# Optimization experiments

Hardware: AMD Instinct MI355X
Metric: run time of the kernel (lower is better)

Reference implementation:

```python
import jax, jax.numpy as jnp
import numpy as np

COMMITMENT = 1.0


def setup_inputs() -> dict:
    key = jax.random.key(0)
    k1, k2 = jax.random.split(key)
    input = jax.random.normal(k1, (8, 64, 64, 256), dtype=jnp.float32)
    embed = jax.random.normal(k2, (256, 8192), dtype=jnp.float32)  # [dim, n_embed]
    return {"input": input, "embed": embed}


def reference(input, embed):
    dim = embed.shape[0]
    flatten = input.reshape(-1, dim)  # [N, dim]
    dist = (
        jnp.sum(flatten * flatten, axis=1, keepdims=True)
        - 2.0 * (flatten @ embed)
        + jnp.sum(embed * embed, axis=0, keepdims=True)
    )
    embed_ind = jnp.argmin(dist, axis=1)  # == (-dist).max(1) indices
    embed_ind = embed_ind.reshape(input.shape[:-1])  # [B, H, W]
    quantize = jnp.take(embed.T, embed_ind, axis=0)  # codebook lookup [B,H,W,dim]
    loss = jnp.mean((jax.lax.stop_gradient(quantize) - input) ** 2) * COMMITMENT
    quantize = input + jax.lax.stop_gradient(quantize - input)  # straight-through
    return quantize, embed_ind, loss
```

## Files before the change

kernel.cpp:

```cpp
#include <hip/hip_runtime.h>
#include <hip/hip_fp16.h>

#define NROW 32768
#define DIM  256
#define NC   8192
#define CAP  16384
#define MARGINF 0.25f
#define BIAS 512.0f
#define AST 576
#define BST 576
#define LOSS_SCALE (1.0f / 8388608.0f)

typedef __attribute__((ext_vector_type(8))) _Float16 half8;
typedef __attribute__((ext_vector_type(4))) _Float16 half4;
typedef __attribute__((ext_vector_type(4))) float   floatx4;
typedef const __attribute__((address_space(1))) void* gas_p;
typedef __attribute__((address_space(3))) void*       las_p;

static __device__ __forceinline__ unsigned short f2hb(float f) {
    _Float16 h = (_Float16)f;
    unsigned short u;
    __builtin_memcpy(&u, &h, 2);
    return u;
}
static __device__ __forceinline__ unsigned umin_(unsigned a, unsigned b) { return a < b ? a : b; }
static __device__ __forceinline__ unsigned umax_(unsigned a, unsigned b) { return a > b ? a : b; }


__global__ void prep_a_k(const float* __restrict__ x, unsigned short* __restrict__ Ah,
                         float* __restrict__ norms) {
    int row  = blockIdx.x * 4 + (threadIdx.x >> 6);
    int lane = threadIdx.x & 63;
    const float4 v = ((const float4*)(x + (size_t)row * DIM))[lane];
    float s = v.x * v.x + v.y * v.y + v.z * v.z + v.w * v.w;
#pragma unroll
    for (int off = 32; off; off >>= 1) s += __shfl_down(s, off, 64);
    if (lane == 0) norms[row] = s;
    ushort4 hi4 = make_ushort4(f2hb(v.x), f2hb(v.y), f2hb(v.z), f2hb(v.w));
    ushort4 lo4 = make_ushort4(f2hb(v.x - (float)(_Float16)v.x),
                               f2hb(v.y - (float)(_Float16)v.y),
                               f2hb(v.z - (float)(_Float16)v.z),
                               f2hb(v.w - (float)(_Float16)v.w));
    unsigned short* rp = Ah + (size_t)row * AST;
    *(ushort4*)(rp + lane * 4)       = hi4;
    *(ushort4*)(rp + 288 + lane * 4) = lo4;
    if (lane < 8) {
        ushort4 ob = make_ushort4(0, 0, 0, 0);
        if (lane == 0) { ob.x = 0x3C00; ob.y = 0x3C00; }
        *(ushort4*)(rp + 256 + lane * 4) = ob;
    }
}

__global__ void code_norms_k(const float* __restrict__ e, unsigned short* __restrict__ Bh,
                             float* __restrict__ cHalf) {
    int j = blockIdx.x * 256 + threadIdx.x;
    float s = 0.f;
    for (int d = 0; d < DIM; ++d) { float v = e[(size_t)d * NC + j]; s += v * v; }
    cHalf[j] = 0.5f * s;
    float t = -0.5f * s - BIAS;
    unsigned short hi = f2hb(t);
    _Float16 hf; __builtin_memcpy(&hf, &hi, 2);
    unsigned short lo = f2hb(t - (float)hf);
    unsigned short* p = Bh + (size_t)j * BST + 256;
    p[0] = hi; p[1] = lo;
    for (int k2 = 2; k2 < 32; ++k2) p[k2] = 0;
}

__global__ void prep_b_k(const float* __restrict__ e, unsigned short* __restrict__ Bh) {
    __shared__ float t[32][33];
    int jb = blockIdx.x * 32, db = blockIdx.y * 32;
#pragma unroll
    for (int i = 0; i < 4; ++i)
        t[threadIdx.y + i * 8][threadIdx.x] =
            e[(size_t)(db + threadIdx.y + i * 8) * NC + jb + threadIdx.x];
    __syncthreads();
#pragma unroll
    for (int i = 0; i < 4; ++i) {
        int j = jb + threadIdx.y + i * 8;
        int d = db + threadIdx.x;
        float val = t[threadIdx.x][threadIdx.y + i * 8];
        Bh[(size_t)j * BST + d]       = f2hb(val);
        Bh[(size_t)j * BST + 288 + d] = f2hb(val - (float)(_Float16)val);
    }
}


#define WAITBAR asm volatile("s_waitcnt vmcnt(2) lgkmcnt(4)\n\ts_barrier" ::: "memory")

__global__ __launch_bounds__(512, 2) void vq_cheap_k(
    const unsigned short* __restrict__ Ah, const unsigned short* __restrict__ Bh,
    const float* __restrict__ cHalf,
    float* __restrict__ pv, int* __restrict__ pj, float* __restrict__ psv)
{
    __shared__ __align__(16) _Float16 Asl[8][4096];
    __shared__ __align__(16) _Float16 Bsl[4][8192];
    __shared__ float chl[2048];

    const int tid  = threadIdx.x;
    const int js   = blockIdx.x & 3;
    const int rb   = blockIdx.x >> 2;
    const int row0 = rb * 128, col0 = js * 2048;
    const int lane = tid & 63, l15 = lane & 15, lq = lane >> 4;
    const int wave = tid >> 6;
    const int wr = (wave >> 2) * 64;
    const int wc = (wave & 3) * 64;
    const int sr = tid >> 2;
    const int ks = (((tid & 3) ^ (sr & 3) ^ ((sr >> 2) & 3))) * 8;

    {
        float4 a = ((const float4*)(cHalf + col0))[tid];
        a.x += BIAS; a.y += BIAS; a.z += BIAS; a.w += BIAS;
        ((float4*)chl)[tid] = a;
    }

    const unsigned short* Abase = Ah + (size_t)(row0 + sr) * AST + ks;
#pragma unroll
    for (int c = 0; c < 8; ++c)
        __builtin_amdgcn_global_load_lds((gas_p)(Abase + c * 32), (las_p)&Asl[c][tid * 8], 16, 0, 0);

#define LOADB(JT_, C_, BUF_)                                                                  \
    do {                                                                                      \
        const unsigned short* bb_ = Bh + (size_t)(col0 + (JT_) * 256 + sr) * BST + (C_) * 32 + ks; \
        _Float16* lb_ = &Bsl[(BUF_)][tid * 8];                                                \
        __builtin_amdgcn_global_load_lds((gas_p)bb_,               (las_p)lb_,          16, 0, 0); \
        __builtin_amdgcn_global_load_lds((gas_p)(bb_ + 128 * BST), (las_p)(lb_ + 4096), 16, 0, 0); \
    } while (0)

    LOADB(0, 0, 0);
    LOADB(0, 1, 1);
    LOADB(0, 2, 2);

    unsigned k1[16], k2[16];
#pragma unroll
    for (int s = 0; s < 16; ++s) { k1[s] = 0xFFFFFFFFu; k2[s] = 0xFFFFFFFFu; }

    const floatx4 fzero = {0.0f, 0.0f, 0.0f, 0.0f};
    floatx4 acc[4][4];
#pragma unroll
    for (int rf = 0; rf < 4; ++rf)
#pragma unroll
        for (int cf = 0; cf < 4; ++cf) acc[rf][cf] = fzero;

    WAITBAR;

    half8 ar[4][4];
#pragma unroll
    for (int c = 0; c < 4; ++c)
#pragma unroll
        for (int rf = 0; rf < 4; ++rf) {
            const int m = wr + rf * 16 + l15;
            const int g = lq ^ (m & 3) ^ ((m >> 2) & 3);
            ar[c][rf] = *(const half8*)&Asl[c][m * 32 + g * 8];
        }

    half8 af[4], bf[4];
#pragma unroll
    for (int cf = 0; cf < 4; ++cf) {
        const int n = wc + cf * 16 + l15;
        const int g = lq ^ (n & 3) ^ ((n >> 2) & 3);
        bf[cf] = *(const half8*)&Bsl[0][n * 32 + g * 8];
    }

    for (int jt = 0; jt < 8; ++jt) {
#pragma unroll
        for (int c = 0; c < 8; ++c) {
            if (c <= 4) LOADB(jt, c + 3, (c + 3) & 3);
            else        LOADB((jt + 1) & 7, c - 5, (c + 3) & 3);

            __builtin_amdgcn_s_setprio(1);
            if (c < 4) {
#pragma unroll
                for (int rf = 0; rf < 4; ++rf)
#pragma unroll
                    for (int cf = 0; cf < 4; ++cf)
                        acc[rf][cf] = __builtin_amdgcn_mfma_f32_16x16x32_f16(
                            ar[c][rf], bf[cf], acc[rf][cf], 0, 0, 0);
            } else {
#pragma unroll
                for (int rf = 0; rf < 4; ++rf)
#pragma unroll
                    for (int cf = 0; cf < 4; ++cf)
                        acc[rf][cf] = __builtin_amdgcn_mfma_f32_16x16x32_f16(
                            af[rf], bf[cf], acc[rf][cf], 0, 0, 0);
            }
            __builtin_amdgcn_s_setprio(0);
            __builtin_amdgcn_sched_barrier(0);

            if (c == 7) {
#pragma unroll
                for (int cf = 0; cf < 4; ++cf) {
                    const unsigned colb = (unsigned)(jt * 256 + wc + cf * 16 + l15);
                    const float ch = chl[colb];
#pragma unroll
                    for (int rf = 0; rf < 4; ++rf)
#pragma unroll
                        for (int r = 0; r < 4; ++r) {
                            float s = acc[rf][cf][r] - ch;
                            unsigned key = (__float_as_uint(s) & 0xFFFFF800u) | colb;
                            int slot = rf * 4 + r;
                            unsigned t = umax_(key, k1[slot]);
                            k1[slot] = umin_(k1[slot], key);
                            k2[slot] = umin_(k2[slot], t);
                        }
                }
#pragma unroll
                for (int rf = 0; rf < 4; ++rf)
#pragma unroll
                    for (int cf = 0; cf < 4; ++cf) acc[rf][cf] = fzero;
            }

            if (((c + 1) & 7) >= 4) {
#pragma unroll
                for (int rf = 0; rf < 4; ++rf) {
                    const int m = wr + rf * 16 + l15;
                    const int g = lq ^ (m & 3) ^ ((m >> 2) & 3);
                    af[rf] = *(const half8*)&Asl[(c + 1) & 7][m * 32 + g * 8];
                }
            }
#pragma unroll
            for (int cf = 0; cf < 4; ++cf) {
                const int n = wc + cf * 16 + l15;
                const int g = lq ^ (n & 3) ^ ((n >> 2) & 3);
                bf[cf] = *(const half8*)&Bsl[(c + 1) & 3][n * 32 + g * 8];
            }

            WAITBAR;
        }
    }
#undef LOADB

#pragma unroll
    for (int st = 1; st < 16; st <<= 1) {
#pragma unroll
        for (int s = 0; s < 16; ++s) {
            unsigned o1 = (unsigned)__shfl_xor((int)k1[s], st, 64);
            unsigned o2 = (unsigned)__shfl_xor((int)k2[s], st, 64);
            unsigned t = umax_(k1[s], o1);
            k1[s] = umin_(k1[s], o1);
            k2[s] = umin_(umin_(k2[s], o2), t);
        }
    }

    __syncthreads();
    unsigned* mk1 = (unsigned*)&Asl[0][0];
    unsigned* mk2 = (unsigned*)&Asl[1][0];
    if (l15 == 0) {
#pragma unroll
        for (int rf = 0; rf < 4; ++rf)
#pragma unroll
            for (int r = 0; r < 4; ++r) {
                int rloc = wr + rf * 16 + lq * 4 + r;
                int slot = rf * 4 + r;
                mk1[rloc * 4 + (wave & 3)] = k1[slot];
                mk2[rloc * 4 + (wave & 3)] = k2[slot];
            }
    }
    __syncthreads();
    if (tid < 128) {
        unsigned a0 = mk1[tid * 4], a1 = mk1[tid * 4 + 1], a2 = mk1[tid * 4 + 2], a3 = mk1[tid * 4 + 3];
        unsigned x = umin_(a0, a1), y = umax_(a0, a1);
        unsigned z = umin_(a2, a3), w = umax_(a2, a3);
        unsigned m1  = umin_(x, z);
        unsigned sm1 = umin_(umax_(x, z), umin_(y, w));
        unsigned s0 = mk2[tid * 4], s1 = mk2[tid * 4 + 1], s2 = mk2[tid * 4 + 2], s3 = mk2[tid * 4 + 3];
        unsigned m2 = umin_(umin_(umin_(s0, s1), umin_(s2, s3)), sm1);
        pv[(size_t)js * NROW + row0 + tid]  = __uint_as_float(m1 & 0xFFFFF800u);
        pj[(size_t)js * NROW + row0 + tid]  = (int)(m1 & 2047u) + js * 2048;
        psv[(size_t)js * NROW + row0 + tid] = __uint_as_float(m2 & 0xFFFFF800u);
    }
}

#undef WAITBAR


template<bool RESCUE>
static __device__ __forceinline__ void chunk_off(int c, int& ac, int& bc) {
    if constexpr (RESCUE) {
        if (c < 8)       { ac = c * 32;              bc = c * 32; }
        else if (c < 16) { ac = (c - 8) * 32;        bc = 288 + (c - 8) * 32; }
        else             { ac = 288 + (c - 16) * 32; bc = (c - 16) * 32; }
    } else {
        ac = c * 32; bc = c * 32;
    }
}

#define GWAIT asm volatile("s_waitcnt vmcnt(4) lgkmcnt(0)\n\ts_barrier" ::: "memory")

template<int CHUNKS, int JT, int JSB, bool RESCUE>
__global__ __launch_bounds__(256, 2) void vq_gemm_k(
    const unsigned short* __restrict__ Ah, const unsigned short* __restrict__ Bh,
    const float* __restrict__ cHalf,
    float* __restrict__ pv, int* __restrict__ pj, float* __restrict__ psv,
    const int* __restrict__ list, const int* __restrict__ cnt)
{
    static_assert(CHUNKS % 3 == 0, "3-deep ring requires CHUNKS % 3 == 0");
    __shared__ __align__(16) _Float16 As[3][4096];
    __shared__ __align__(16) _Float16 Bs[3][4096];

    const int tid  = threadIdx.x;
    const int js   = blockIdx.x & ((1 << JSB) - 1);
    const int rb   = blockIdx.x >> JSB;
    const int row0 = rb * 128, col0 = js * (JT * 128);
    const int lane = tid & 63, l15 = lane & 15, lq = lane >> 4;
    const int wave = tid >> 6;
    const int wrow = (wave >> 1) * 64, wcol = (wave & 1) * 64;
    const int sr = tid >> 2, sp = (tid & 3) * 8;

    int nact = 0;
    if constexpr (RESCUE) {
        nact = *cnt;
        if (row0 >= nact) return;
    }

    const unsigned short *Abase0, *Abase1;
    if constexpr (RESCUE) {
        int i0 = row0 + sr, i1 = i0 + 64;
        int r0 = (i0 < nact) ? list[i0] : 0;
        int r1 = (i1 < nact) ? list[i1] : 0;
        Abase0 = Ah + (size_t)r0 * AST + sp;
        Abase1 = Ah + (size_t)r1 * AST + sp;
    } else {
        Abase0 = Ah + (size_t)(row0 + sr) * AST + sp;
        Abase1 = Abase0 + 64 * AST;
    }

    unsigned k1[16], k2[16];
    float bvf[16]; int bjf[16];
#pragma unroll
    for (int s = 0; s < 16; ++s) {
        k1[s] = 0xFFFFFFFFu; k2[s] = 0xFFFFFFFFu;
        bvf[s] = -3.4e38f; bjf[s] = 0;
    }

    const floatx4 fzero = {0.0f, 0.0f, 0.0f, 0.0f};
    floatx4 acc[4][4];
#pragma unroll
    for (int rf = 0; rf < 4; ++rf)
#pragma unroll
        for (int cf = 0; cf < 4; ++cf) acc[rf][cf] = fzero;

    const unsigned short* Bb0 = Bh + (size_t)(col0 + sr) * BST + sp;

#define LOAD4T(JT_, C_)                                                                      \
    do {                                                                                     \
        int an_, bn_;                                                                        \
        chunk_off<RESCUE>((C_), an_, bn_);                                                   \
        const unsigned short* bb_ = Bb0 + (size_t)(JT_) * (128 * BST);                       \
        _Float16* la_ = &As[(C_) % 3][tid * 8];                                              \
        _Float16* lb_ = &Bs[(C_) % 3][tid * 8];                                              \
        __builtin_amdgcn_global_load_lds((gas_p)(Abase0 + an_),            (las_p)la_,          16, 0, 0); \
        __builtin_amdgcn_global_load_lds((gas_p)(Abase1 + an_),            (las_p)(la_ + 2048), 16, 0, 0); \
        __builtin_amdgcn_global_load_lds((gas_p)(bb_ + bn_),               (las_p)lb_,          16, 0, 0); \
        __builtin_amdgcn_global_load_lds((gas_p)(bb_ + 64 * BST + bn_),    (las_p)(lb_ + 2048), 16, 0, 0); \
    } while (0)

    LOAD4T(0, 0);
    LOAD4T(0, 1);

    for (int jt = 0; jt < JT; ++jt) {
#pragma unroll
        for (int c = 0; c < CHUNKS; ++c) {
            GWAIT;
            if (c + 2 < CHUNKS)       LOAD4T(jt, c + 2);
            else if (jt + 1 < JT)     LOAD4T(jt + 1, c + 2 - CHUNKS);

            half8 af[4], bf[4];
#pragma unroll
            for (int rf = 0; rf < 4; ++rf)
                af[rf] = *(const half8*)&As[c % 3][(wrow + rf * 16 + l15) * 32 + lq * 8];
#pragma unroll
            for (int cf = 0; cf < 4; ++cf)
                bf[cf] = *(const half8*)&Bs[c % 3][(wcol + cf * 16 + l15) * 32 + lq * 8];
#pragma unroll
            for (int rf = 0; rf < 4; ++rf)
#pragma unroll
                for (int cf = 0; cf < 4; ++cf)
                    acc[rf][cf] = __builtin_amdgcn_mfma_f32_16x16x32_f16(
                        af[rf], bf[cf], acc[rf][cf], 0, 0, 0);

            if (c == CHUNKS - 1) {
                if constexpr (RESCUE) {
                    const int colbase = col0 + jt * 128 + wcol;
#pragma unroll
                    for (int cf = 0; cf < 4; ++cf) {
                        const int col = colbase + cf * 16 + l15;
                        const float ch = cHalf[col];
#pragma unroll
                        for (int rf = 0; rf < 4; ++rf)
#pragma unroll
                            for (int r = 0; r < 4; ++r) {
                                float s = acc[rf][cf][r] - ch;
                                int slot = rf * 4 + r;
                                if (s > bvf[slot]) { bvf[slot] = s; bjf[slot] = col; }
                            }
                    }
                } else {
                    const unsigned colloc = (unsigned)(jt * 128 + wcol);
#pragma unroll
                    for (int cf = 0; cf < 4; ++cf) {
                        const unsigned colb = colloc + cf * 16 + l15;
#pragma unroll
                        for (int rf = 0; rf < 4; ++rf)
#pragma unroll
                            for (int r = 0; r < 4; ++r) {
                                unsigned key = (__float_as_uint(acc[rf][cf][r]) & 0xFFFFF800u) | colb;
                                int slot = rf * 4 + r;
                                unsigned t = umax_(key, k1[slot]);
                                k1[slot] = umin_(k1[slot], key);
                                k2[slot] = umin_(k2[slot], t);
                            }
                    }
                }
#pragma unroll
                for (int rf = 0; rf < 4; ++rf)
#pragma unroll
                    for (int cf = 0; cf < 4; ++cf) acc[rf][cf] = fzero;
            }
        }
    }
#undef LOAD4T

#pragma unroll
    for (int st = 1; st < 16; st <<= 1) {
#pragma unroll
        for (int s = 0; s < 16; ++s) {
            if constexpr (RESCUE) {
                float v2 = __shfl_xor(bvf[s], st, 64);
                int   j2 = __shfl_xor(bjf[s], st, 64);
                if (v2 > bvf[s] || (v2 == bvf[s] && j2 < bjf[s])) { bvf[s] = v2; bjf[s] = j2; }
            } else {
                unsigned o1 = (unsigned)__shfl_xor((int)k1[s], st, 64);
                unsigned o2 = (unsigned)__shfl_xor((int)k2[s], st, 64);
                unsigned t = umax_(k1[s], o1);
                k1[s] = umin_(k1[s], o1);
                k2[s] = umin_(umin_(k2[s], o2), t);
            }
        }
    }

    __syncthreads();
    if constexpr (RESCUE) {
        float* mv = (float*)&As[0][0];
        int*   mj = (int*)&Bs[0][0];
        if (l15 == 0) {
#pragma unroll
            for (int rf = 0; rf < 4; ++rf)
#pragma unroll
                for (int r = 0; r < 4; ++r) {
                    int rloc = wrow + rf * 16 + lq * 4 + r;
                    int slot = rf * 4 + r;
                    mv[rloc * 2 + (wave & 1)] = bvf[slot];
                    mj[rloc * 2 + (wave & 1)] = bjf[slot];
                }
        }
        __syncthreads();
        if (tid < 128) {
            float v0 = mv[tid * 2], v1 = mv[tid * 2 + 1];
            int   j0 = mj[tid * 2], j1 = mj[tid * 2 + 1];
            bool take1 = (v1 > v0) || (v1 == v0 && j1 < j0);
            pv[(size_t)js * CAP + row0 + tid] = take1 ? v1 : v0;
            pj[(size_t)js * CAP + row0 + tid] = take1 ? j1 : j0;
        }
    } else {
        unsigned* mk1 = (unsigned*)&As[0][0];
        unsigned* mk2 = (unsigned*)&Bs[0][0];
        if (l15 == 0) {
#pragma unroll
            for (int rf = 0; rf < 4; ++rf)
#pragma unroll
                for (int r = 0; r < 4; ++r) {
                    int rloc = wrow + rf * 16 + lq * 4 + r;
                    int slot = rf * 4 + r;
                    mk1[rloc * 2 + (wave & 1)] = k1[slot];
                    mk2[rloc * 2 + (wave & 1)] = k2[slot];
                }
        }
        __syncthreads();
        if (tid < 128) {
            unsigned a1 = mk1[tid * 2], b1 = mk1[tid * 2 + 1];
            unsigned a2 = mk2[tid * 2], b2 = mk2[tid * 2 + 1];
            unsigned m1 = umin_(a1, b1);
            unsigned m2 = umin_(umin_(a2, b2), umax_(a1, b1));
            pv[(size_t)js * NROW + row0 + tid] = __uint_as_float(m1 & 0xFFFFF800u);
            pj[(size_t)js * NROW + row0 + tid] = (int)(m1 & 2047u) + js * (JT * 128);
            psv[(size_t)js * NROW + row0 + tid] = __uint_as_float(m2 & 0xFFFFF800u);
        }
    }
}


__global__ void vq_reduce_k(const float* __restrict__ pv, const int* __restrict__ pj,
                            const float* __restrict__ psv,
                            const float* __restrict__ norms, const unsigned short* __restrict__ Bh,
                            float* __restrict__ qout, float* __restrict__ iout,
                            float* __restrict__ lout, int* __restrict__ list,
                            int* __restrict__ cnt)
{
    __shared__ int jbuf[64];
    const int row0 = blockIdx.x * 64;
    const int tid = threadIdx.x;
    if (tid < 64) {
        int row = row0 + tid;
        float bv = pv[row]; int bj = pj[row]; float sv = psv[row];
#pragma unroll
        for (int s = 1; s < 4; ++s) {
            float v = pv[(size_t)s * NROW + row];
            int   j = pj[(size_t)s * NROW + row];
            float s2 = psv[(size_t)s * NROW + row];
            bool better = (v > bv) || (v == bv && j < bj);
            float loseBest = better ? bv : v;
            sv = fmaxf(fmaxf(sv, s2), loseBest);
            if (better) { bv = v; bj = j; }
        }
        bool flagged = (bv - sv) < MARGINF;
        if (flagged) {
            int idx = atomicAdd(cnt, 1);
            if (idx < CAP) {
                list[idx] = row;
                jbuf[tid] = -1;
            } else {
                flagged = false;
            }
        }
        float rl = 0.f;
        if (!flagged) {
            iout[row] = (float)bj;
            jbuf[tid] = bj;
            rl = norms[row] - 2.0f * (bv + BIAS - 0.0625f);
        }
#pragma unroll
        for (int off = 32; off; off >>= 1) rl += __shfl_down(rl, off, 64);
        if (tid == 0) atomicAdd(lout, rl * LOSS_SCALE);
    }
    __syncthreads();
    const int lane = tid & 63;
    for (int r = tid >> 6; r < 64; r += 4) {
        int j = jbuf[r];
        if (j >= 0) {
            const _Float16* bp = (const _Float16*)Bh + (size_t)j * BST + lane * 4;
            half4 h = *(const half4*)bp;
            half4 l = *(const half4*)(bp + 288);
            float4 v;
            v.x = (float)h[0] + (float)l[0];
            v.y = (float)h[1] + (float)l[1];
            v.z = (float)h[2] + (float)l[2];
            v.w = (float)h[3] + (float)l[3];
            *(float4*)&qout[(size_t)(row0 + r) * DIM + lane * 4] = v;
        }
    }
}


__global__ void vq_reduce2_k(const float* __restrict__ pv2, const int* __restrict__ pj2,
                             const int* __restrict__ list, const int* __restrict__ cnt,
                             const float* __restrict__ norms, const unsigned short* __restrict__ Bh,
                             float* __restrict__ qout, float* __restrict__ iout,
                             float* __restrict__ lout)
{
    __shared__ int rbuf[64], jb2[64];
    const int n = *cnt < CAP ? *cnt : CAP;
    const int i0 = blockIdx.x * 64;
    if (i0 >= n) return;
    const int tid = threadIdx.x;
    if (tid < 64) {
        int i = i0 + tid;
        float rl = 0.f;
        if (i < n) {
            float bv = pv2[i]; int bj = pj2[i];
#pragma unroll 4
            for (int s = 1; s < 32; ++s) {
                float v = pv2[(size_t)s * CAP + i];
                int   j = pj2[(size_t)s * CAP + i];
                if (v > bv || (v == bv && j < bj)) { bv = v; bj = j; }
            }
            int row = list[i];
            iout[row] = (float)bj;
            rbuf[tid] = row;
            jb2[tid]  = bj;
            rl = norms[row] - 2.0f * bv;
        } else {
            rbuf[tid] = -1;
        }
#pragma unroll
        for (int off = 32; off; off >>= 1) rl += __shfl_down(rl, off, 64);
        if (tid == 0) atomicAdd(lout, rl * LOSS_SCALE);
    }
    __syncthreads();
    const int lane = tid & 63;
    for (int r = tid >> 6; r < 64; r += 4) {
        int row = rbuf[r];
        if (row >= 0) {
            const _Float16* bp = (const _Float16*)Bh + (size_t)jb2[r] * BST + lane * 4;
            half4 h = *(const half4*)bp;
            half4 l = *(const half4*)(bp + 288);
            float4 v;
            v.x = (float)h[0] + (float)l[0];
            v.y = (float)h[1] + (float)l[1];
            v.z = (float)h[2] + (float)l[2];
            v.w = (float)h[3] + (float)l[3];
            *(float4*)&qout[(size_t)row * DIM + lane * 4] = v;
        }
    }
}


__global__ void transpose_k(const float* __restrict__ e, float* __restrict__ eT) {
    __shared__ float t[32][33];
    int jb = blockIdx.x * 32, db = blockIdx.y * 32;
#pragma unroll
    for (int i = 0; i < 4; ++i)
        t[threadIdx.y + i * 8][threadIdx.x] =
            e[(size_t)(db + threadIdx.y + i * 8) * NC + jb + threadIdx.x];
    __syncthreads();
#pragma unroll
    for (int i = 0; i < 4; ++i)
        eT[(size_t)(jb + threadIdx.y + i * 8) * DIM + db + threadIdx.x] =
            t[threadIdx.x][threadIdx.y + i * 8];
}

__global__ void row_norms_k(const float* __restrict__ x, float* __restrict__ norms) {
    int row  = blockIdx.x * 4 + (threadIdx.x >> 6);
    int lane = threadIdx.x & 63;
    const float4 v = ((const float4*)(x + (size_t)row * DIM))[lane];
    float s = v.x * v.x + v.y * v.y + v.z * v.z + v.w * v.w;
#pragma unroll
    for (int off = 32; off; off >>= 1) s += __shfl_down(s, off, 64);
    if (lane == 0) norms[row] = s;
}

__global__ void code_norms_fb_k(const float* __restrict__ e, float* __restrict__ cHalf) {
    int j = blockIdx.x * 256 + threadIdx.x;
    float s = 0.f;
    for (int d = 0; d < DIM; ++d) { float v = e[(size_t)d * NC + j]; s += v * v; }
    cHalf[j] = 0.5f * s;
}

__global__ __launch_bounds__(256, 4) void vq_main_k(
    const float* __restrict__ x, const float* __restrict__ e,
    const float* __restrict__ eT, const float* __restrict__ norms,
    const float* __restrict__ cHalf, float* __restrict__ qout,
    float* __restrict__ iout, float* __restrict__ lout, int useT)
{
    __shared__ float  As[2][32 * 68];
    __shared__ float4 Bs[2][512];
    const int tid  = threadIdx.x;
    const int row0 = blockIdx.x * 64;
    const int ty = tid >> 4, tx = tid & 15;
    const int ar = tid >> 2, ak = (tid & 3) * 4;
    const int bk = tid >> 4, bj = tid & 15;
    float bestv[4]; int bestj[4];
#pragma unroll
    for (int i = 0; i < 4; ++i) { bestv[i] = -3.4e38f; bestj[i] = 0; }
    float acc[4][4];
    float4 pa0, pa1, pb0, pb1;
    {
        const float* xp = x + (size_t)(row0 + ar) * DIM + ak;
        pa0 = *(const float4*)xp;
        pa1 = *(const float4*)(xp + 16);
        const float* ep = e + (size_t)bk * NC + bj * 4;
        pb0 = *(const float4*)ep;
        pb1 = *(const float4*)(ep + 16 * NC);
    }
    int buf = 0;
    for (int c = 0; c < 1024; ++c) {
        const int kc = c & 7;
#pragma unroll
        for (int q = 0; q < 4; ++q) As[buf][(ak + q) * 68 + ar]      = ((const float*)&pa0)[q];
#pragma unroll
        for (int q = 0; q < 4; ++q) As[buf][(16 + ak + q) * 68 + ar] = ((const float*)&pa1)[q];
        Bs[buf][bk * 16 + bj]        = pb0;
        Bs[buf][(bk + 16) * 16 + bj] = pb1;
        __syncthreads();
        if (c + 1 < 1024) {
            int j0n  = ((c + 1) >> 3) * 64;
            int kk0n = ((c + 1) & 7) * 32;
            const float* xp = x + (size_t)(row0 + ar) * DIM + kk0n + ak;
            pa0 = *(const float4*)xp;
            pa1 = *(const float4*)(xp + 16);
            const float* ep = e + (size_t)(kk0n + bk) * NC + j0n + bj * 4;
            pb0 = *(const float4*)ep;
            pb1 = *(const float4*)(ep + 16 * NC);
        }
        if (kc == 0) {
#pragma unroll
            for (int i = 0; i < 4; ++i)
#pragma unroll
                for (int j = 0; j < 4; ++j) acc[i][j] = 0.f;
        }
#pragma unroll
        for (int k = 0; k < 32; ++k) {
            float4 a = *(const float4*)&As[buf][k * 68 + ty * 4];
            float4 b = *(const float4*)&Bs[buf][k * 16 + tx];
            acc[0][0] += a.x * b.x; acc[0][1] += a.x * b.y; acc[0][2] += a.x * b.z; acc[0][3] += a.x * b.w;
            acc[1][0] += a.y * b.x; acc[1][1] += a.y * b.y; acc[1][2] += a.y * b.z; acc[1][3] += a.y * b.w;
            acc[2][0] += a.z * b.x; acc[2][1] += a.z * b.y; acc[2][2] += a.z * b.z; acc[2][3] += a.z * b.w;
            acc[3][0] += a.w * b.x; acc[3][1] += a.w * b.y; acc[3][2] += a.w * b.z; acc[3][3] += a.w * b.w;
        }
        if (kc == 7) {
            int j0 = (c >> 3) * 64;
            float4 ch = *(const float4*)&cHalf[j0 + tx * 4];
            int jb0 = j0 + tx * 4;
#pragma unroll
            for (int i = 0; i < 4; ++i)
#pragma unroll
                for (int j = 0; j < 4; ++j) {
                    float s = acc[i][j] - ((const float*)&ch)[j];
                    if (s > bestv[i]) { bestv[i] = s; bestj[i] = jb0 + j; }
                }
        }
        buf ^= 1;
    }
    __syncthreads();
    float* redv   = &As[0][0];
    int*   redj   = (int*)&As[0][1024];
    int*   idxbuf = (int*)&As[1][0];
#pragma unroll
    for (int i = 0; i < 4; ++i) {
        int r = ty * 4 + i;
        redv[r * 16 + tx] = bestv[i];
        redj[r * 16 + tx] = bestj[i];
    }
    __syncthreads();
    if (tid < 64) {
        float bvv = redv[tid * 16];
        int   bj2 = redj[tid * 16];
#pragma unroll
        for (int t = 1; t < 16; ++t) {
            float v = redv[tid * 16 + t];
            int   j = redj[tid * 16 + t];
            if (v > bvv || (v == bvv && j < bj2)) { bvv = v; bj2 = j; }
        }
        iout[row0 + tid] = (float)bj2;
        idxbuf[tid] = bj2;
        float rl = norms[row0 + tid] - 2.0f * bvv;
#pragma unroll
        for (int off = 32; off; off >>= 1) rl += __shfl_down(rl, off, 64);
        if (tid == 0) atomicAdd(lout, rl * LOSS_SCALE);
    }
    __syncthreads();
    {
        const int rr = tid >> 6, lane = tid & 63;
        for (int r = rr; r < 64; r += 4) {
            int j = idxbuf[r];
            float4 v;
            if (useT) {
                v = *(const float4*)&eT[(size_t)j * DIM + lane * 4];
            } else {
                int d = lane * 4;
                v.x = e[(size_t)d * NC + j];
                v.y = e[(size_t)(d + 1) * NC + j];
                v.z = e[(size_t)(d + 2) * NC + j];
                v.w = e[(size_t)(d + 3) * NC + j];
            }
            *(float4*)&qout[(size_t)(row0 + r) * DIM + lane * 4] = v;
        }
    }
}


extern "C" void kernel_launch(void* const* d_in, const int* in_sizes, int n_in,
                              void* d_out, int out_size, void* d_ws, size_t ws_size,
                              hipStream_t stream) {
    const float* x = (const float*)d_in[0];
    const float* e = (const float*)d_in[1];

    float* qout = (float*)d_out;
    float* iout = qout + (size_t)NROW * DIM;
    float* lout = iout + NROW;

    char* ws = (char*)d_ws;
    const size_t offAh    = 0;
    const size_t offBh    = offAh + 37748736;
    const size_t offNorms = offBh + 9437184;
    const size_t offCH    = offNorms + 131072;
    const size_t offPV    = offCH + 32768;
    const size_t offPJ    = offPV + 524288;
    const size_t offPSV   = offPJ + 524288;
    const size_t offPV2   = offPSV + 524288;
    const size_t offPJ2   = offPV2 + 2097152;
    const size_t offList  = offPJ2 + 2097152;
    const size_t offCnt   = offList + 65536;
    const size_t needFast = offCnt + 256;

    hipMemsetAsync(lout, 0, sizeof(float), stream);

    if (ws_size >= needFast) {
        unsigned short* Ah = (unsigned short*)(ws + offAh);
        unsigned short* Bh = (unsigned short*)(ws + offBh);
        float* norms = (float*)(ws + offNorms);
        float* cHalf = (float*)(ws + offCH);
        float* pv    = (float*)(ws + offPV);
        int*   pj    = (int*)(ws + offPJ);
        float* psv   = (float*)(ws + offPSV);
        float* pv2   = (float*)(ws + offPV2);
        int*   pj2   = (int*)(ws + offPJ2);
        int*   list  = (int*)(ws + offList);
        int*   cnt   = (int*)(ws + offCnt);

        hipMemsetAsync(cnt, 0, sizeof(int), stream);
        prep_a_k<<<NROW / 4, 256, 0, stream>>>(x, Ah, norms);
        code_norms_k<<<NC / 256, 256, 0, stream>>>(e, Bh, cHalf);
        prep_b_k<<<dim3(NC / 32, DIM / 32), dim3(32, 8), 0, stream>>>(e, Bh);
        vq_cheap_k<<<1024, 512, 0, stream>>>(Ah, Bh, cHalf, pv, pj, psv);
        vq_reduce_k<<<NROW / 64, 256, 0, stream>>>(
            pv, pj, psv, norms, Bh, qout, iout, lout, list, cnt);
        vq_gemm_k<24, 2, 5, true><<<(CAP / 128) * 32, 256, 0, stream>>>(
            Ah, Bh, cHalf, pv2, pj2, nullptr, list, cnt);
        vq_reduce2_k<<<CAP / 64, 256, 0, stream>>>(
            pv2, pj2, list, cnt, norms, Bh, qout, iout, lout);
    } else {
        float* fws   = (float*)d_ws;
        float* norms = fws;
        float* cHalf = fws + NROW;
        float* eT    = fws + NROW + NC;
        size_t need_T = (size_t)(NROW + NC) * sizeof(float) + (size_t)NC * DIM * sizeof(float);
        int useT = (ws_size >= need_T) ? 1 : 0;
        row_norms_k<<<NROW / 4, 256, 0, stream>>>(x, norms);
        code_norms_fb_k<<<NC / 256, 256, 0, stream>>>(e, cHalf);
        if (useT)
            transpose_k<<<dim3(NC / 32, DIM / 32), dim3(32, 8), 0, stream>>>(e, eT);
        vq_main_k<<<NROW / 64, 256, 0, stream>>>(x, e, eT, norms, cHalf, qout, iout, lout, useT);
    }
}
```

Before: 343.7 us.

## Shrink cheap-GEMM tile to 64 rows with wave-private B staging, no barriers

Result: slower. 378.5 us (+10.1%).

```diff
diff --git a/kernel.cpp b/kernel.cpp
--- a/kernel.cpp
+++ b/kernel.cpp
@@ -85,27 +85,22 @@
 }
 
 
-#define WAITBAR asm volatile("s_waitcnt vmcnt(2) lgkmcnt(4)\n\ts_barrier" ::: "memory")
-
-__global__ __launch_bounds__(512, 2) void vq_cheap_k(
+__global__ __launch_bounds__(512, 4) void vq_cheap_k(
     const unsigned short* __restrict__ Ah, const unsigned short* __restrict__ Bh,
     const float* __restrict__ cHalf,
     float* __restrict__ pv, int* __restrict__ pj, float* __restrict__ psv)
 {
-    __shared__ __align__(16) _Float16 Asl[8][4096];
-    __shared__ __align__(16) _Float16 Bsl[4][8192];
+    __shared__ __align__(16) _Float16 Asl[8][2048];
+    __shared__ __align__(16) _Float16 Bsl[2][8192];
     __shared__ float chl[2048];
 
     const int tid  = threadIdx.x;
     const int js   = blockIdx.x & 3;
     const int rb   = blockIdx.x >> 2;
-    const int row0 = rb * 128, col0 = js * 2048;
+    const int row0 = rb * 64, col0 = js * 2048;
     const int lane = tid & 63, l15 = lane & 15, lq = lane >> 4;
     const int wave = tid >> 6;
-    const int wr = (wave >> 2) * 64;
-    const int wc = (wave & 3) * 64;
-    const int sr = tid >> 2;
-    const int ks = (((tid & 3) ^ (sr & 3) ^ ((sr >> 2) & 3))) * 8;
+    const int wc   = wave * 32;
 
     {
         float4 a = ((const float4*)(cHalf + col0))[tid];
@@ -113,121 +108,121 @@
         ((float4*)chl)[tid] = a;
     }
 
-    const unsigned short* Abase = Ah + (size_t)(row0 + sr) * AST + ks;
-#pragma unroll
-    for (int c = 0; c < 8; ++c)
-        __builtin_amdgcn_global_load_lds((gas_p)(Abase + c * 32), (las_p)&Asl[c][tid * 8], 16, 0, 0);
-
-#define LOADB(JT_, C_, BUF_)                                                                  \
+#pragma unroll
+    for (int q = 0; q < 4; ++q) {
+        const int idx = q * 512 + tid;
+        const int ck  = idx >> 8;
+        const int r   = (idx >> 2) & 63;
+        const int gp  = idx & 3;
+        const int g   = gp ^ ((r & 3) ^ ((r >> 2) & 3));
+        __builtin_amdgcn_global_load_lds(
+            (gas_p)(Ah + (size_t)(row0 + r) * AST + ck * 32 + g * 8),
+            (las_p)((_Float16*)Asl + (size_t)idx * 8), 16, 0, 0);
+    }
+
+    const int colq = wc + ((lane >> 2) & 15);
+    const int gq   = ((lane & 3) ^ ((colq & 3) ^ ((colq >> 2) & 3))) * 8;
+    const unsigned short* Bq0 = Bh + (size_t)(col0 + colq) * BST + gq;
+    const unsigned short* Bq1 = Bq0 + 16 * BST;
+
+#define STAGEB(JT_, C_, SLOT_)                                                                \
     do {                                                                                      \
-        const unsigned short* bb_ = Bh + (size_t)(col0 + (JT_) * 256 + sr) * BST + (C_) * 32 + ks; \
-        _Float16* lb_ = &Bsl[(BUF_)][tid * 8];                                                \
-        __builtin_amdgcn_global_load_lds((gas_p)bb_,               (las_p)lb_,          16, 0, 0); \
-        __builtin_amdgcn_global_load_lds((gas_p)(bb_ + 128 * BST), (las_p)(lb_ + 4096), 16, 0, 0); \
+        const size_t off_ = (size_t)(JT_) * (256 * BST) + (C_) * 32;                          \
+        __builtin_amdgcn_global_load_lds((gas_p)(Bq0 + off_),                                 \
+            (las_p)(&Bsl[(SLOT_)][wc * 32] + lane * 8), 16, 0, 0);                            \
+        __builtin_amdgcn_global_load_lds((gas_p)(Bq1 + off_),                                 \
+            (las_p)(&Bsl[(SLOT_)][(wc + 16) * 32] + lane * 8), 16, 0, 0);                     \
     } while (0)
 
-    LOADB(0, 0, 0);
-    LOADB(0, 1, 1);
-    LOADB(0, 2, 2);
+    STAGEB(0, 0, 0);
+    STAGEB(0, 1, 1);
 
     unsigned k1[16], k2[16];
 #pragma unroll
     for (int s = 0; s < 16; ++s) { k1[s] = 0xFFFFFFFFu; k2[s] = 0xFFFFFFFFu; }
 
     const floatx4 fzero = {0.0f, 0.0f, 0.0f, 0.0f};
-    floatx4 acc[4][4];
+    floatx4 acc[4][2];
 #pragma unroll
     for (int rf = 0; rf < 4; ++rf)
 #pragma unroll
-        for (int cf = 0; cf < 4; ++cf) acc[rf][cf] = fzero;
-
-    WAITBAR;
-
-    half8 ar[4][4];
-#pragma unroll
-    for (int c = 0; c < 4; ++c)
-#pragma unroll
-        for (int rf = 0; rf < 4; ++rf) {
-            const int m = wr + rf * 16 + l15;
-            const int g = lq ^ (m & 3) ^ ((m >> 2) & 3);
-            ar[c][rf] = *(const half8*)&Asl[c][m * 32 + g * 8];
-        }
-
-    half8 af[4], bf[4];
-#pragma unroll
-    for (int cf = 0; cf < 4; ++cf) {
+        for (int cf = 0; cf < 2; ++cf) acc[rf][cf] = fzero;
+
+    asm volatile("s_waitcnt vmcnt(0) lgkmcnt(0)" ::: "memory");
+    __builtin_amdgcn_s_barrier();
+
+    half8 af[4], bf[2];
+#pragma unroll
+    for (int rf = 0; rf < 4; ++rf) {
+        const int m = rf * 16 + l15;
+        const int g = lq ^ ((m & 3) ^ ((m >> 2) & 3));
+        af[rf] = *(const half8*)&Asl[0][m * 32 + g * 8];
+    }
+#pragma unroll
+    for (int cf = 0; cf < 2; ++cf) {
         const int n = wc + cf * 16 + l15;
-        const int g = lq ^ (n & 3) ^ ((n >> 2) & 3);
+        const int g = lq ^ ((n & 3) ^ ((n >> 2) & 3));
         bf[cf] = *(const half8*)&Bsl[0][n * 32 + g * 8];
     }
 
     for (int jt = 0; jt < 8; ++jt) {
 #pragma unroll
         for (int c = 0; c < 8; ++c) {
-            if (c <= 4) LOADB(jt, c + 3, (c + 3) & 3);
-            else        LOADB((jt + 1) & 7, c - 5, (c + 3) & 3);
-
             __builtin_amdgcn_s_setprio(1);
-            if (c < 4) {
-#pragma unroll
-                for (int rf = 0; rf < 4; ++rf)
-#pragma unroll
-                    for (int cf = 0; cf < 4; ++cf)
-                        acc[rf][cf] = __builtin_amdgcn_mfma_f32_16x16x32_f16(
-                            ar[c][rf], bf[cf], acc[rf][cf], 0, 0, 0);
-            } else {
-#pragma unroll
-                for (int rf = 0; rf < 4; ++rf)
-#pragma unroll
-                    for (int cf = 0; cf < 4; ++cf)
-                        acc[rf][cf] = __builtin_amdgcn_mfma_f32_16x16x32_f16(
-                            af[rf], bf[cf], acc[rf][cf], 0, 0, 0);
-            }
+#pragma unroll
+            for (int rf = 0; rf < 4; ++rf)
+#pragma unroll
+                for (int cf = 0; cf < 2; ++cf)
+                    acc[rf][cf] = __builtin_amdgcn_mfma_f32_16x16x32_f16(
+                        af[rf], bf[cf], acc[rf][cf], 0, 0, 0);
             __builtin_amdgcn_s_setprio(0);
             __builtin_amdgcn_sched_barrier(0);
 
             if (c == 7) {
 #pragma unroll
-                for (int cf = 0; cf < 4; ++cf) {
+                for (int cf = 0; cf < 2; ++cf) {
                     const unsigned colb = (unsigned)(jt * 256 + wc + cf * 16 + l15);
-                    const float ch = chl[colb];
+                    const float chv = chl[colb];
 #pragma unroll
                     for (int rf = 0; rf < 4; ++rf)
 #pragma unroll
                         for (int r = 0; r < 4; ++r) {
-                            float s = acc[rf][cf][r] - ch;
+                            float s = acc[rf][cf][r] - chv;
                             unsigned key = (__float_as_uint(s) & 0xFFFFF800u) | colb;
-                            int slot = rf * 4 + r;
-                            unsigned t = umax_(key, k1[slot]);
-                            k1[slot] = umin_(k1[slot], key);
-                            k2[slot] = umin_(k2[slot], t);
+                            int sl = rf * 4 + r;
+                            unsigned t = umax_(key, k1[sl]);
+                            k1[sl] = umin_(k1[sl], key);
+                            k2[sl] = umin_(k2[sl], t);
                         }
                 }
 #pragma unroll
                 for (int rf = 0; rf < 4; ++rf)
 #pragma unroll
-                    for (int cf = 0; cf < 4; ++cf) acc[rf][cf] = fzero;
-            }
-
-            if (((c + 1) & 7) >= 4) {
-#pragma unroll
-                for (int rf = 0; rf < 4; ++rf) {
-                    const int m = wr + rf * 16 + l15;
-                    const int g = lq ^ (m & 3) ^ ((m >> 2) & 3);
-                    af[rf] = *(const half8*)&Asl[(c + 1) & 7][m * 32 + g * 8];
-                }
-            }
-#pragma unroll
-            for (int cf = 0; cf < 4; ++cf) {
+                    for (int cf = 0; cf < 2; ++cf) acc[rf][cf] = fzero;
+            }
+
+            {
+                const int T = (jt * 8 + c + 2) & 63;
+                STAGEB(T >> 3, T & 7, c & 1);
+            }
+
+            asm volatile("s_waitcnt vmcnt(2)" ::: "memory");
+
+#pragma unroll
+            for (int rf = 0; rf < 4; ++rf) {
+                const int m = rf * 16 + l15;
+                const int g = lq ^ ((m & 3) ^ ((m >> 2) & 3));
+                af[rf] = *(const half8*)&Asl[(c + 1) & 7][m * 32 + g * 8];
+            }
+#pragma unroll
+            for (int cf = 0; cf < 2; ++cf) {
                 const int n = wc + cf * 16 + l15;
-                const int g = lq ^ (n & 3) ^ ((n >> 2) & 3);
-                bf[cf] = *(const half8*)&Bsl[(c + 1) & 3][n * 32 + g * 8];
-            }
-
-            WAITBAR;
-        }
-    }
-#undef LOADB
+                const int g = lq ^ ((n & 3) ^ ((n >> 2) & 3));
+                bf[cf] = *(const half8*)&Bsl[(c + 1) & 1][n * 32 + g * 8];
+            }
+        }
+    }
+#undef STAGEB
 
 #pragma unroll
     for (int st = 1; st < 16; st <<= 1) {
@@ -243,34 +238,35 @@
 
     __syncthreads();
     unsigned* mk1 = (unsigned*)&Asl[0][0];
-    unsigned* mk2 = (unsigned*)&Asl[1][0];
+    unsigned* mk2 = (unsigned*)&Asl[2][0];
     if (l15 == 0) {
 #pragma unroll
         for (int rf = 0; rf < 4; ++rf)
 #pragma unroll
             for (int r = 0; r < 4; ++r) {
-                int rloc = wr + rf * 16 + lq * 4 + r;
-                int slot = rf * 4 + r;
-                mk1[rloc * 4 + (wave & 3)] = k1[slot];
-                mk2[rloc * 4 + (wave & 3)] = k2[slot];
-            }
-    }
-    __syncthreads();
-    if (tid < 128) {
-        unsigned a0 = mk1[tid * 4], a1 = mk1[tid * 4 + 1], a2 = mk1[tid * 4 + 2], a3 = mk1[tid * 4 + 3];
-        unsigned x = umin_(a0, a1), y = umax_(a0, a1);
-        unsigned z = umin_(a2, a3), w = umax_(a2, a3);
-        unsigned m1  = umin_(x, z);
-        unsigned sm1 = umin_(umax_(x, z), umin_(y, w));
-        unsigned s0 = mk2[tid * 4], s1 = mk2[tid * 4 + 1], s2 = mk2[tid * 4 + 2], s3 = mk2[tid * 4 + 3];
-        unsigned m2 = umin_(umin_(umin_(s0, s1), umin_(s2, s3)), sm1);
-        pv[(size_t)js * NROW + row0 + tid]  = __uint_as_float(m1 & 0xFFFFF800u);
-        pj[(size_t)js * NROW + row0 + tid]  = (int)(m1 & 2047u) + js * 2048;
+                int rloc = rf * 16 + lq * 4 + r;
+                int sl = rf * 4 + r;
+                mk1[rloc * 8 + wave] = k1[sl];
+                mk2[rloc * 8 + wave] = k2[sl];
+            }
+    }
+    __syncthreads();
+    if (tid < 64) {
+        unsigned m = 0xFFFFFFFFu, sm = 0xFFFFFFFFu, q2 = 0xFFFFFFFFu;
+#pragma unroll
+        for (int w = 0; w < 8; ++w) {
+            unsigned v = mk1[tid * 8 + w];
+            unsigned t = umax_(v, m);
+            m  = umin_(m, v);
+            sm = umin_(sm, t);
+            q2 = umin_(q2, mk2[tid * 8 + w]);
+        }
+        unsigned m2 = umin_(q2, sm);
+        pv[(size_t)js * NROW + row0 + tid]  = __uint_as_float(m & 0xFFFFF800u);
+        pj[(size_t)js * NROW + row0 + tid]  = (int)(m & 2047u) + js * 2048;
         psv[(size_t)js * NROW + row0 + tid] = __uint_as_float(m2 & 0xFFFFF800u);
     }
 }
-
-#undef WAITBAR
 
 
 template<bool RESCUE>
@@ -801,7 +797,7 @@
         prep_a_k<<<NROW / 4, 256, 0, stream>>>(x, Ah, norms);
         code_norms_k<<<NC / 256, 256, 0, stream>>>(e, Bh, cHalf);
         prep_b_k<<<dim3(NC / 32, DIM / 32), dim3(32, 8), 0, stream>>>(e, Bh);
-        vq_cheap_k<<<1024, 512, 0, stream>>>(Ah, Bh, cHalf, pv, pj, psv);
+        vq_cheap_k<<<2048, 512, 0, stream>>>(Ah, Bh, cHalf, pv, pj, psv);
         vq_reduce_k<<<NROW / 64, 256, 0, stream>>>(
             pv, pj, psv, norms, Bh, qout, iout, lout, list, cnt);
         vq_gemm_k<24, 2, 5, true><<<(CAP / 128) * 32, 256, 0, stream>>>(
```

## Load codebook fragments directly from global into registers in cheap VQ kernel

Applied to the files above, without the earlier changes.

Measured after the change: 437.8 us. 27.4% more time.

```diff
diff --git a/kernel.cpp b/kernel.cpp
--- a/kernel.cpp
+++ b/kernel.cpp
@@ -85,15 +85,12 @@
 }
 
 
-#define WAITBAR asm volatile("s_waitcnt vmcnt(2) lgkmcnt(4)\n\ts_barrier" ::: "memory")
-
 __global__ __launch_bounds__(512, 2) void vq_cheap_k(
     const unsigned short* __restrict__ Ah, const unsigned short* __restrict__ Bh,
     const float* __restrict__ cHalf,
     float* __restrict__ pv, int* __restrict__ pj, float* __restrict__ psv)
 {
     __shared__ __align__(16) _Float16 Asl[8][4096];
-    __shared__ __align__(16) _Float16 Bsl[4][8192];
     __shared__ float chl[2048];
 
     const int tid  = threadIdx.x;
@@ -118,17 +115,10 @@
     for (int c = 0; c < 8; ++c)
         __builtin_amdgcn_global_load_lds((gas_p)(Abase + c * 32), (las_p)&Asl[c][tid * 8], 16, 0, 0);
 
-#define LOADB(JT_, C_, BUF_)                                                                  \
-    do {                                                                                      \
-        const unsigned short* bb_ = Bh + (size_t)(col0 + (JT_) * 256 + sr) * BST + (C_) * 32 + ks; \
-        _Float16* lb_ = &Bsl[(BUF_)][tid * 8];                                                \
-        __builtin_amdgcn_global_load_lds((gas_p)bb_,               (las_p)lb_,          16, 0, 0); \
-        __builtin_amdgcn_global_load_lds((gas_p)(bb_ + 128 * BST), (las_p)(lb_ + 4096), 16, 0, 0); \
-    } while (0)
-
-    LOADB(0, 0, 0);
-    LOADB(0, 1, 1);
-    LOADB(0, 2, 2);
+    const unsigned short* Bb0 = Bh + (size_t)(col0 + wc +  0 + l15) * BST + lq * 8;
+    const unsigned short* Bb1 = Bh + (size_t)(col0 + wc + 16 + l15) * BST + lq * 8;
+    const unsigned short* Bb2 = Bh + (size_t)(col0 + wc + 32 + l15) * BST + lq * 8;
+    const unsigned short* Bb3 = Bh + (size_t)(col0 + wc + 48 + l15) * BST + lq * 8;
 
     unsigned k1[16], k2[16];
 #pragma unroll
@@ -141,61 +131,63 @@
 #pragma unroll
         for (int cf = 0; cf < 4; ++cf) acc[rf][cf] = fzero;
 
-    WAITBAR;
-
-    half8 ar[4][4];
-#pragma unroll
-    for (int c = 0; c < 4; ++c)
-#pragma unroll
-        for (int rf = 0; rf < 4; ++rf) {
-            const int m = wr + rf * 16 + l15;
-            const int g = lq ^ (m & 3) ^ ((m >> 2) & 3);
-            ar[c][rf] = *(const half8*)&Asl[c][m * 32 + g * 8];
-        }
-
-    half8 af[4], bf[4];
-#pragma unroll
-    for (int cf = 0; cf < 4; ++cf) {
-        const int n = wc + cf * 16 + l15;
-        const int g = lq ^ (n & 3) ^ ((n >> 2) & 3);
-        bf[cf] = *(const half8*)&Bsl[0][n * 32 + g * 8];
+    asm volatile("s_waitcnt vmcnt(0) lgkmcnt(0)" ::: "memory");
+    __builtin_amdgcn_s_barrier();
+
+    half8 af2[2][4], bf2[2][4];
+    bf2[0][0] = *(const half8*)(Bb0);
+    bf2[0][1] = *(const half8*)(Bb1);
+    bf2[0][2] = *(const half8*)(Bb2);
+    bf2[0][3] = *(const half8*)(Bb3);
+#pragma unroll
+    for (int rf = 0; rf < 4; ++rf) {
+        const int m = wr + rf * 16 + l15;
+        const int g = lq ^ (m & 3) ^ ((m >> 2) & 3);
+        af2[0][rf] = *(const half8*)&Asl[0][m * 32 + g * 8];
     }
 
     for (int jt = 0; jt < 8; ++jt) {
 #pragma unroll
         for (int c = 0; c < 8; ++c) {
-            if (c <= 4) LOADB(jt, c + 3, (c + 3) & 3);
-            else        LOADB((jt + 1) & 7, c - 5, (c + 3) & 3);
+            const int cur = c & 1;
+            const int nxt = cur ^ 1;
+            const int cn  = (c + 1) & 7;
+            const int jtn = (c == 7) ? ((jt + 1) & 7) : jt;
+
+            {
+                const size_t boff = (size_t)jtn * (256 * BST) + (size_t)cn * 32;
+                bf2[nxt][0] = *(const half8*)(Bb0 + boff);
+                bf2[nxt][1] = *(const half8*)(Bb1 + boff);
+                bf2[nxt][2] = *(const half8*)(Bb2 + boff);
+                bf2[nxt][3] = *(const half8*)(Bb3 + boff);
+            }
+#pragma unroll
+            for (int rf = 0; rf < 4; ++rf) {
+                const int m = wr + rf * 16 + l15;
+                const int g = lq ^ (m & 3) ^ ((m >> 2) & 3);
+                af2[nxt][rf] = *(const half8*)&Asl[cn][m * 32 + g * 8];
+            }
+            __builtin_amdgcn_sched_barrier(0);
 
             __builtin_amdgcn_s_setprio(1);
-            if (c < 4) {
-#pragma unroll
-                for (int rf = 0; rf < 4; ++rf)
-#pragma unroll
-                    for (int cf = 0; cf < 4; ++cf)
-                        acc[rf][cf] = __builtin_amdgcn_mfma_f32_16x16x32_f16(
-                            ar[c][rf], bf[cf], acc[rf][cf], 0, 0, 0);
-            } else {
-#pragma unroll
-                for (int rf = 0; rf < 4; ++rf)
-#pragma unroll
-                    for (int cf = 0; cf < 4; ++cf)
-                        acc[rf][cf] = __builtin_amdgcn_mfma_f32_16x16x32_f16(
-                            af[rf], bf[cf], acc[rf][cf], 0, 0, 0);
-            }
+#pragma unroll
+            for (int rf = 0; rf < 4; ++rf)
+#pragma unroll
+                for (int cf = 0; cf < 4; ++cf)
+                    acc[rf][cf] = __builtin_amdgcn_mfma_f32_16x16x32_f16(
+                        af2[cur][rf], bf2[cur][cf], acc[rf][cf], 0, 0, 0);
             __builtin_amdgcn_s_setprio(0);
-            __builtin_amdgcn_sched_barrier(0);
 
             if (c == 7) {
 #pragma unroll
                 for (int cf = 0; cf < 4; ++cf) {
                     const unsigned colb = (unsigned)(jt * 256 + wc + cf * 16 + l15);
-                    const float ch = chl[colb];
+                    const float chv = chl[colb];
 #pragma unroll
                     for (int rf = 0; rf < 4; ++rf)
 #pragma unroll
                         for (int r = 0; r < 4; ++r) {
-                            float s = acc[rf][cf][r] - ch;
+                            float s = acc[rf][cf][r] - chv;
                             unsigned key = (__float_as_uint(s) & 0xFFFFF800u) | colb;
                             int slot = rf * 4 + r;
                             unsigned t = umax_(key, k1[slot]);
@@ -208,26 +200,8 @@
 #pragma unroll
                     for (int cf = 0; cf < 4; ++cf) acc[rf][cf] = fzero;
             }
-
-            if (((c + 1) & 7) >= 4) {
-#pragma unroll
-                for (int rf = 0; rf < 4; ++rf) {
-                    const int m = wr + rf * 16 + l15;
-                    const int g = lq ^ (m & 3) ^ ((m >> 2) & 3);
-                    af[rf] = *(const half8*)&Asl[(c + 1) & 7][m * 32 + g * 8];
-                }
-            }
-#pragma unroll
-            for (int cf = 0; cf < 4; ++cf) {
-                const int n = wc + cf * 16 + l15;
-                const int g = lq ^ (n & 3) ^ ((n >> 2) & 3);
-                bf[cf] = *(const half8*)&Bsl[(c + 1) & 3][n * 32 + g * 8];
-            }
-
-            WAITBAR;
-        }
-    }
-#undef LOADB
+        }
+    }
 
 #pragma unroll
     for (int st = 1; st < 16; st <<= 1) {
@@ -269,8 +243,6 @@
         psv[(size_t)js * NROW + row0 + tid] = __uint_as_float(m2 & 0xFFFFF800u);
     }
 }
-
-#undef WAITBAR
 
 
 template<bool RESCUE>
```
